# Performance work log

Hardware: AMD Instinct MI355X
Metric: run time of the kernel (lower is better)

The kernel has to match this reference:

```python
import jax, jax.numpy as jnp
import numpy as np

CHUNKS = 4
QMAX = 127.0

def fake_quant_int8(t):
    # per-tensor amax calibration -> symmetric int8 fake quant with STE
    amax = jnp.max(jnp.abs(t))
    scale = jnp.maximum(amax, 1e-12) / QMAX
    q = jnp.clip(jnp.round(t / scale), -128.0, 127.0) * scale
    return t + jax.lax.stop_gradient(q - t)

def conv2d(x, w):
    # NCHW x, OIHW w; stride 1, padding 1, dilation 1, groups 1
    return jax.lax.conv_general_dilated(
        x, w, window_strides=(1, 1), padding=((1, 1), (1, 1)),
        dimension_numbers=('NCHW', 'OIHW', 'NCHW'))

def setup_inputs() -> dict:
    key = jax.random.key(0)
    k1, k2, k3 = jax.random.split(key, 3)
    x = jax.random.normal(k1, (8, 256, 128, 128), dtype=jnp.float32)
    weight = jax.random.normal(k2, (512, 256, 3, 3), dtype=jnp.float32) * 0.05
    bias_data = jax.random.normal(k3, (512,), dtype=jnp.float32)
    return {'x': x, 'weight': weight, 'bias_data': bias_data}

def reference(x, weight, bias_data):
    # seg_mode='weight', opt_type='default': input quantized once,
    # weight chunked along out_channels, each chunk quantized separately.
    xq = fake_quant_int8(x)
    out_ch = weight.shape[0]
    csize = out_ch // CHUNKS
    outs = []
    for i in range(CHUNKS):
        w_chunk = weight[i * csize:(i + 1) * csize]
        wq = fake_quant_int8(w_chunk)
        outs.append(conv2d(xq, wq))
    res = jnp.concatenate(outs, axis=1)  # [B, out_ch, H, W]
    return res + bias_data[None, :, None, None]
```

## Files before the change

### kernel.cpp

```cpp
#include <hip/hip_runtime.h>
#include <hip/hip_bf16.h>


typedef int i32x4 __attribute__((ext_vector_type(4)));

__device__ __forceinline__ void llds16(const void* g, void* l) {
    __builtin_amdgcn_global_load_lds(
        (const __attribute__((address_space(1))) void*)g,
        (__attribute__((address_space(3))) void*)l,
        16, 0, 0);
}

__device__ __forceinline__ float f4max(float4 v) {
    return fmaxf(fmaxf(fabsf(v.x), fabsf(v.y)), fmaxf(fabsf(v.z), fabsf(v.w)));
}

__global__ __launch_bounds__(256) void k_amax(const float4* __restrict__ x,
                                              const float4* __restrict__ w4,
                                              float* __restrict__ part) {
    __shared__ float red[4];
    int t = threadIdx.x;
    float m = 0.f;
    if (blockIdx.x < 2048) {
        int tid = blockIdx.x * 256 + t;
        float4 v[16];
#pragma unroll
        for (int k = 0; k < 16; ++k)
            v[k] = x[(size_t)tid + (size_t)k * 524288];
#pragma unroll
        for (int k = 0; k < 16; ++k) m = fmaxf(m, f4max(v[k]));
    } else {
        int b = blockIdx.x - 2048;
        int chunk = b / 288;
        int tid = (b - chunk * 288) * 256 + t;
        m = f4max(w4[(size_t)chunk * 73728 + tid]);
    }
    for (int off = 32; off > 0; off >>= 1) m = fmaxf(m, __shfl_xor(m, off, 64));
    if ((t & 63) == 0) red[t >> 6] = m;
    __syncthreads();
    if (t == 0)
        part[blockIdx.x] = fmaxf(fmaxf(red[0], red[1]), fmaxf(red[2], red[3]));
}

__global__ __launch_bounds__(256) void k_amax2(const float* __restrict__ part,
                                               unsigned* __restrict__ amaxb) {
    __shared__ float red[4];
    int t = threadIdx.x;
    float m = 0.f;
#pragma unroll
    for (int k = 0; k < 8; ++k) m = fmaxf(m, part[t + k * 256]);
    for (int off = 32; off > 0; off >>= 1) m = fmaxf(m, __shfl_xor(m, off, 64));
    if ((t & 63) == 0) red[t >> 6] = m;
    __syncthreads();
    if (t == 0)
        amaxb[0] = __float_as_uint(fmaxf(fmaxf(red[0], red[1]), fmaxf(red[2], red[3])));
    int c = t >> 6, l = t & 63;
    float wm = 0.f;
#pragma unroll
    for (int k = 0; k < 5; ++k) {
        int i = l + k * 64;
        if (i < 288) wm = fmaxf(wm, part[2048 + c * 288 + i]);
    }
    for (int off = 32; off > 0; off >>= 1) wm = fmaxf(wm, __shfl_xor(wm, off, 64));
    if (l == 0) amaxb[1 + c] = __float_as_uint(wm);
}

__global__ __launch_bounds__(256) void k_quant_x(const float* __restrict__ x,
                                                 signed char* __restrict__ qx,
                                                 const unsigned* __restrict__ amaxb) {
    float inv = 127.0f / fmaxf(__uint_as_float(amaxb[0]), 1e-12f);
    int row = blockIdx.x;
    int n = row >> 7, h = row & 127;
    int t = threadIdx.x;
    int w4 = t & 31, cg = t >> 5;
    const float* base = x + (size_t)n * 256 * 16384 + (size_t)h * 128 + w4 * 4;
#pragma unroll
    for (int pp = 0; pp < 2; ++pp) {
        int c0 = pp * 128 + cg * 16;
        float4 v[16];
#pragma unroll
        for (int j = 0; j < 16; ++j)
            v[j] = *(const float4*)(base + (size_t)(c0 + j) * 16384);
#pragma unroll
        for (int i = 0; i < 4; ++i) {
            unsigned wds[4];
#pragma unroll
            for (int jg = 0; jg < 4; ++jg) {
                unsigned u = 0;
#pragma unroll
                for (int jj = 0; jj < 4; ++jj) {
                    float f = (&v[jg * 4 + jj].x)[i];
                    int q = (int)fminf(fmaxf(rintf(f * inv), -128.f), 127.f);
                    u |= ((unsigned)(q & 255)) << (8 * jj);
                }
                wds[jg] = u;
            }
            *(uint4*)&qx[(size_t)row * 32768 + (size_t)(w4 * 4 + i) * 256 + c0] =
                make_uint4(wds[0], wds[1], wds[2], wds[3]);
        }
    }
}

__global__ void k_quant_w(const float* __restrict__ wsrc, signed char* __restrict__ qw,
                          const unsigned* __restrict__ amaxb) {
    int idx = blockIdx.x * 256 + threadIdx.x;
    int oc = idx >> 8, c = idx & 255;
    float inv = 127.0f / fmaxf(__uint_as_float(amaxb[1 + (oc >> 7)]), 1e-12f);
    const float* src = wsrc + (size_t)idx * 9;
    float v[9];
#pragma unroll
    for (int rs = 0; rs < 9; ++rs) v[rs] = src[rs];
#pragma unroll
    for (int rs = 0; rs < 9; ++rs) {
        float qf = fminf(fmaxf(rintf(v[rs] * inv), -128.f), 127.f);
        qw[((size_t)(rs * 512 + oc)) * 256 + c] = (signed char)(int)qf;
    }
}

__global__ __launch_bounds__(256, 2) void k_conv(
    const signed char* __restrict__ qx, const signed char* __restrict__ qw,
    const signed char* __restrict__ zb, const unsigned* __restrict__ amaxb,
    const float* __restrict__ bias, float* __restrict__ out) {
    __shared__ __align__(16) signed char xs[4 * 8320];
    __shared__ __align__(16) signed char wt[3 * 128 * 64];
    int orig = blockIdx.x;
    int wgid = (orig & 7) * 256 + (orig >> 3);
    int rowpair = wgid >> 2, ocg = wgid & 3;
    int n = rowpair >> 6;
    int h0 = (rowpair & 63) * 2;
    int t = threadIdx.x, wid = t >> 6, lane = t & 63;
    int p = lane & 15, hi = lane >> 4;
    int rowsel = wid >> 1, whalf = wid & 1;

    i32x4 acc[8][4] = {};

    auto stageX = [&](int cb) {
#pragma unroll
        for (int i = 0; i < 9; ++i) {
            int idx = t + i * 256;
            if (idx < 2080) {
                int rowk = idx / 520;
                int j = idx - rowk * 520;
                int wr = j >> 2, q4 = j & 3;
                int wg = wr - 1;
                int hh = h0 - 1 + rowk;
                int q4s = q4 ^ ((wr >> 1) & 3);
                const signed char* src = (hh >= 0 && hh < 128 && wg >= 0 && wg < 128)
                    ? qx + (size_t)(n * 128 + hh) * 32768 + wg * 256 + cb * 64 + q4s * 16
                    : zb;
                llds16(src, xs + (size_t)(i * 256 + wid * 64) * 16);
            }
        }
    };
    auto stageW = [&](int cb, int r) {
#pragma unroll
        for (int i = 0; i < 6; ++i) {
            int idx = t + i * 256;
            int s = idx >> 9, rem = idx & 511;
            int oc = rem >> 2, q4 = rem & 3;
            int q4s = q4 ^ ((oc >> 1) & 3);
            const signed char* src = qw
                + (size_t)((r * 3 + s) * 512 + ocg * 128 + oc) * 256 + cb * 64 + q4s * 16;
            llds16(src, wt + (size_t)(i * 256 + wid * 64) * 16);
        }
    };

    for (int cb = 0; cb < 4; ++cb) {
#pragma unroll
        for (int r = 0; r < 3; ++r) {
            if (r == 0) stageX(cb);
            stageW(cb, r);
            __syncthreads();
            int rowk = r + rowsel;
#pragma unroll
            for (int s = 0; s < 3; ++s) {
                i32x4 a[8], b[4];
#pragma unroll
                for (int mf = 0; mf < 8; ++mf) {
                    int ocr = mf * 16 + p;
                    a[mf] = *(const i32x4*)&wt[s * 8192 + ocr * 64
                                               + ((hi ^ ((ocr >> 1) & 3)) << 4)];
                }
#pragma unroll
                for (int nf = 0; nf < 4; ++nf) {
                    int wrow = whalf * 64 + nf * 16 + p + s;
                    b[nf] = *(const i32x4*)&xs[rowk * 8320 + wrow * 64
                                               + ((hi ^ ((wrow >> 1) & 3)) << 4)];
                }
#pragma unroll
                for (int mf = 0; mf < 8; ++mf)
#pragma unroll
                    for (int nf = 0; nf < 4; ++nf)
                        acc[mf][nf] = __builtin_amdgcn_mfma_i32_16x16x64_i8(
                            a[mf], b[nf], acc[mf][nf], 0, 0, 0);
            }
            __syncthreads();
        }
    }

    float sx = fmaxf(__uint_as_float(amaxb[0]), 1e-12f) / 127.0f;
    float sw = fmaxf(__uint_as_float(amaxb[1 + ocg]), 1e-12f) / 127.0f;
    float sc = sx * sw;
    int h = h0 + rowsel;
#pragma unroll
    for (int mf = 0; mf < 8; ++mf)
#pragma unroll
        for (int nf = 0; nf < 4; ++nf)
#pragma unroll
            for (int j = 0; j < 4; ++j) {
                int oc = ocg * 128 + mf * 16 + hi * 4 + j;
                int px = whalf * 64 + nf * 16 + p;
                out[((size_t)(n * 512 + oc) * 128 + h) * 128 + px] =
                    (float)acc[mf][nf][j] * sc + bias[oc];
            }
}

extern "C" void kernel_launch(void* const* d_in, const int* in_sizes, int n_in,
                              void* d_out, int out_size, void* d_ws, size_t ws_size,
                              hipStream_t stream) {
    const float* x    = (const float*)d_in[0];
    const float* wgt  = (const float*)d_in[1];
    const float* bias = (const float*)d_in[2];
    float* out = (float*)d_out;

    unsigned* amaxb = (unsigned*)d_ws;
    float* part = (float*)((char*)d_ws + 256);
    signed char* qx = (signed char*)d_ws + 16384;
    signed char* qw = (signed char*)d_ws + 16384 + 33554432;
    const signed char* zb = (const signed char*)d_ws + 64;

    hipMemsetAsync(d_ws, 0, 256, stream);

    k_amax<<<3200, 256, 0, stream>>>((const float4*)x, (const float4*)wgt, part);
    k_amax2<<<1, 256, 0, stream>>>(part, amaxb);
    k_quant_x<<<1024, 256, 0, stream>>>(x, qx, amaxb);
    k_quant_w<<<512, 256, 0, stream>>>(wgt, qw, amaxb);
    k_conv<<<dim3(2048), 256, 0, stream>>>(qx, qw, zb, amaxb, bias, out);
}
```

Before: 224.2 us.

## Double-buffer conv LDS staging with 512-thread blocks over four output rows

The int8 conv kernel now runs 512-thread workgroups covering four output rows, so each block loads six input rows per channel block instead of four per two rows, which cuts halo re-reads. Input and weight tiles are double-buffered in LDS, with the next stage's global-to-LDS loads issued before computing the current one and gated by explicit vmcnt waits and raw s_barrier. Halo columns are zeroed once at the start, and MFMA sections are wrapped in s_setprio. LDS use roughly doubles, to about 148 KB per block, which may limit occupancy. The hand-tuned vmcnt counts are fragile and could race if they are off.

```diff
diff --git a/kernel.cpp b/kernel.cpp
--- a/kernel.cpp
+++ b/kernel.cpp
@@ -13,6 +13,12 @@
 
 __device__ __forceinline__ float f4max(float4 v) {
     return fmaxf(fmaxf(fabsf(v.x), fabsf(v.y)), fmaxf(fabsf(v.z), fabsf(v.w)));
+}
+
+__device__ __forceinline__ void barrier_f() {
+    asm volatile("" ::: "memory");
+    __builtin_amdgcn_s_barrier();
+    asm volatile("" ::: "memory");
 }
 
 __global__ __launch_bounds__(256) void k_amax(const float4* __restrict__ x,
@@ -117,85 +123,93 @@
     }
 }
 
-__global__ __launch_bounds__(256, 2) void k_conv(
+__global__ __launch_bounds__(512, 2) void k_conv(
     const signed char* __restrict__ qx, const signed char* __restrict__ qw,
     const signed char* __restrict__ zb, const unsigned* __restrict__ amaxb,
     const float* __restrict__ bias, float* __restrict__ out) {
-    __shared__ __align__(16) signed char xs[4 * 8320];
-    __shared__ __align__(16) signed char wt[3 * 128 * 64];
+    __shared__ __align__(16) signed char xs2[2 * 6 * 130 * 64];
+    __shared__ __align__(16) signed char wt2[2 * 3 * 128 * 64];
     int orig = blockIdx.x;
-    int wgid = (orig & 7) * 256 + (orig >> 3);
-    int rowpair = wgid >> 2, ocg = wgid & 3;
-    int n = rowpair >> 6;
-    int h0 = (rowpair & 63) * 2;
+    int wgid = (orig & 7) * 128 + (orig >> 3);
+    int n = wgid >> 7;
+    int rq = (wgid >> 2) & 31, ocg = wgid & 3;
+    int h0 = rq * 4;
     int t = threadIdx.x, wid = t >> 6, lane = t & 63;
-    int p = lane & 15, hi = lane >> 4;
+    int lp = lane & 15, hi = lane >> 4;
     int rowsel = wid >> 1, whalf = wid & 1;
 
     i32x4 acc[8][4] = {};
 
-    auto stageX = [&](int cb) {
-#pragma unroll
-        for (int i = 0; i < 9; ++i) {
-            int idx = t + i * 256;
-            if (idx < 2080) {
-                int rowk = idx / 520;
-                int j = idx - rowk * 520;
-                int wr = j >> 2, q4 = j & 3;
-                int wg = wr - 1;
-                int hh = h0 - 1 + rowk;
-                int q4s = q4 ^ ((wr >> 1) & 3);
-                const signed char* src = (hh >= 0 && hh < 128 && wg >= 0 && wg < 128)
-                    ? qx + (size_t)(n * 128 + hh) * 32768 + wg * 256 + cb * 64 + q4s * 16
-                    : zb;
-                llds16(src, xs + (size_t)(i * 256 + wid * 64) * 16);
-            }
+    auto stageX = [&](int cbx, int bufx) {
+#pragma unroll
+        for (int i = 0; i < 6; ++i) {
+            int hh = h0 - 1 + i;
+            int w = t >> 2, q4 = t & 3;
+            int q4s = q4 ^ (((w + 1) >> 1) & 3);
+            const signed char* src = (hh >= 0 && hh < 128)
+                ? qx + (size_t)(n * 128 + hh) * 32768 + w * 256 + cbx * 64 + q4s * 16
+                : zb;
+            llds16(src, xs2 + (size_t)bufx * 49920 + i * 8320 + 64 + t * 16);
         }
     };
-    auto stageW = [&](int cb, int r) {
-#pragma unroll
-        for (int i = 0; i < 6; ++i) {
-            int idx = t + i * 256;
-            int s = idx >> 9, rem = idx & 511;
-            int oc = rem >> 2, q4 = rem & 3;
+    auto stageW = [&](int cbw, int rw, int bufw) {
+#pragma unroll
+        for (int i = 0; i < 3; ++i) {
+            int oc = t >> 2, q4 = t & 3;
             int q4s = q4 ^ ((oc >> 1) & 3);
             const signed char* src = qw
-                + (size_t)((r * 3 + s) * 512 + ocg * 128 + oc) * 256 + cb * 64 + q4s * 16;
-            llds16(src, wt + (size_t)(i * 256 + wid * 64) * 16);
+                + (size_t)((rw * 3 + i) * 512 + ocg * 128 + oc) * 256 + cbw * 64 + q4s * 16;
+            llds16(src, wt2 + (size_t)bufw * 24576 + i * 8192 + t * 16);
         }
     };
 
-    for (int cb = 0; cb < 4; ++cb) {
-#pragma unroll
-        for (int r = 0; r < 3; ++r) {
-            if (r == 0) stageX(cb);
-            stageW(cb, r);
-            __syncthreads();
-            int rowk = r + rowsel;
-#pragma unroll
-            for (int s = 0; s < 3; ++s) {
-                i32x4 a[8], b[4];
-#pragma unroll
-                for (int mf = 0; mf < 8; ++mf) {
-                    int ocr = mf * 16 + p;
-                    a[mf] = *(const i32x4*)&wt[s * 8192 + ocr * 64
-                                               + ((hi ^ ((ocr >> 1) & 3)) << 4)];
-                }
-#pragma unroll
-                for (int nf = 0; nf < 4; ++nf) {
-                    int wrow = whalf * 64 + nf * 16 + p + s;
-                    b[nf] = *(const i32x4*)&xs[rowk * 8320 + wrow * 64
-                                               + ((hi ^ ((wrow >> 1) & 3)) << 4)];
-                }
-#pragma unroll
-                for (int mf = 0; mf < 8; ++mf)
-#pragma unroll
-                    for (int nf = 0; nf < 4; ++nf)
-                        acc[mf][nf] = __builtin_amdgcn_mfma_i32_16x16x64_i8(
-                            a[mf], b[nf], acc[mf][nf], 0, 0, 0);
-            }
-            __syncthreads();
-        }
+    if (t < 96) {
+        int unit = t >> 2, q = t & 3;
+        int buf = unit / 12, rem = unit % 12;
+        int rowk = rem >> 1, side = rem & 1;
+        *(i32x4*)&xs2[(size_t)buf * 49920 + rowk * 8320 + (side ? 129 : 0) * 64 + q * 16] =
+            i32x4{0, 0, 0, 0};
+    }
+    stageX(0, 0);
+    stageW(0, 0, 0);
+    asm volatile("s_waitcnt lgkmcnt(0)" ::: "memory");
+    barrier_f();
+
+#pragma unroll
+    for (int p = 0; p < 12; ++p) {
+        const int r = p % 3, cb = p / 3;
+        if (p < 11) stageW((p + 1) / 3, (p + 1) % 3, (p + 1) & 1);
+        if (r == 1 && cb < 3) stageX(cb + 1, (cb + 1) & 1);
+        if (p == 11)      asm volatile("s_waitcnt vmcnt(0)" ::: "memory");
+        else if (r == 0 || p == 10) asm volatile("s_waitcnt vmcnt(3)" ::: "memory");
+        else              asm volatile("s_waitcnt vmcnt(9)" ::: "memory");
+        barrier_f();
+        const int wb = p & 1, xb = cb & 1, rowk = r + rowsel;
+#pragma unroll
+        for (int s = 0; s < 3; ++s) {
+            i32x4 a[8], b[4];
+#pragma unroll
+            for (int mf = 0; mf < 8; ++mf) {
+                int ocr = mf * 16 + lp;
+                a[mf] = *(const i32x4*)&wt2[(size_t)wb * 24576 + s * 8192 + ocr * 64
+                                            + ((hi ^ ((ocr >> 1) & 3)) << 4)];
+            }
+#pragma unroll
+            for (int nf = 0; nf < 4; ++nf) {
+                int slot = whalf * 64 + nf * 16 + lp + s;
+                b[nf] = *(const i32x4*)&xs2[(size_t)xb * 49920 + rowk * 8320 + slot * 64
+                                            + ((hi ^ ((slot >> 1) & 3)) << 4)];
+            }
+            __builtin_amdgcn_s_setprio(1);
+#pragma unroll
+            for (int mf = 0; mf < 8; ++mf)
+#pragma unroll
+                for (int nf = 0; nf < 4; ++nf)
+                    acc[mf][nf] = __builtin_amdgcn_mfma_i32_16x16x64_i8(
+                        a[mf], b[nf], acc[mf][nf], 0, 0, 0);
+            __builtin_amdgcn_s_setprio(0);
+        }
+        barrier_f();
     }
 
     float sx = fmaxf(__uint_as_float(amaxb[0]), 1e-12f) / 127.0f;
@@ -209,7 +223,7 @@
 #pragma unroll
             for (int j = 0; j < 4; ++j) {
                 int oc = ocg * 128 + mf * 16 + hi * 4 + j;
-                int px = whalf * 64 + nf * 16 + p;
+                int px = whalf * 64 + nf * 16 + lp;
                 out[((size_t)(n * 512 + oc) * 128 + h) * 128 + px] =
                     (float)acc[mf][nf][j] * sc + bias[oc];
             }
@@ -235,5 +249,5 @@
     k_amax2<<<1, 256, 0, stream>>>(part, amaxb);
     k_quant_x<<<1024, 256, 0, stream>>>(x, qx, amaxb);
     k_quant_w<<<512, 256, 0, stream>>>(wgt, qw, amaxb);
-    k_conv<<<dim3(2048), 256, 0, stream>>>(qx, qw, zb, amaxb, bias, out);
-}
+    k_conv<<<dim3(1024), 512, 0, stream>>>(qx, qw, zb, amaxb, bias, out);
+}
```

Result: slower. 242.0 us (+7.9%).

## Double-buffer per-tap weight tiles and raise occupancy in int8 conv

Applied to the files above, without the earlier changes.

Replaces the three-tap weight staging per kernel row with a two-slot double buffer holding one 3x3 tap at a time. The next tap's weights are prefetched into LDS while the current tap's MFMAs run, and launch bounds rise from 2 to 3 blocks per CU because LDS use drops. The input tile is still loaded synchronously at each channel-block boundary. The cost is more barriers, one per tap instead of one per row, and the higher occupancy target may squeeze the 128 accumulator registers per thread and cause spills.

```diff
diff --git a/kernel.cpp b/kernel.cpp
--- a/kernel.cpp
+++ b/kernel.cpp
@@ -117,19 +117,19 @@
     }
 }
 
-__global__ __launch_bounds__(256, 2) void k_conv(
+__global__ __launch_bounds__(256, 3) void k_conv(
     const signed char* __restrict__ qx, const signed char* __restrict__ qw,
     const signed char* __restrict__ zb, const unsigned* __restrict__ amaxb,
     const float* __restrict__ bias, float* __restrict__ out) {
     __shared__ __align__(16) signed char xs[4 * 8320];
-    __shared__ __align__(16) signed char wt[3 * 128 * 64];
+    __shared__ __align__(16) signed char wt[2][128 * 64];
     int orig = blockIdx.x;
     int wgid = (orig & 7) * 256 + (orig >> 3);
     int rowpair = wgid >> 2, ocg = wgid & 3;
     int n = rowpair >> 6;
     int h0 = (rowpair & 63) * 2;
     int t = threadIdx.x, wid = t >> 6, lane = t & 63;
-    int p = lane & 15, hi = lane >> 4;
+    int lp = lane & 15, hi = lane >> 4;
     int rowsel = wid >> 1, whalf = wid & 1;
 
     i32x4 acc[8][4] = {};
@@ -152,49 +152,54 @@
             }
         }
     };
-    auto stageW = [&](int cb, int r) {
-#pragma unroll
-        for (int i = 0; i < 6; ++i) {
+    auto stageW1 = [&](int P, int buf) {
+        int cb = P / 9, rs = P % 9;
+#pragma unroll
+        for (int i = 0; i < 2; ++i) {
             int idx = t + i * 256;
-            int s = idx >> 9, rem = idx & 511;
-            int oc = rem >> 2, q4 = rem & 3;
+            int oc = idx >> 2, q4 = idx & 3;
             int q4s = q4 ^ ((oc >> 1) & 3);
             const signed char* src = qw
-                + (size_t)((r * 3 + s) * 512 + ocg * 128 + oc) * 256 + cb * 64 + q4s * 16;
-            llds16(src, wt + (size_t)(i * 256 + wid * 64) * 16);
+                + (size_t)(rs * 512 + ocg * 128 + oc) * 256 + cb * 64 + q4s * 16;
+            llds16(src, &wt[buf][0] + (size_t)idx * 16);
         }
     };
 
+    stageX(0);
+    stageW1(0, 0);
+    __syncthreads();
+
     for (int cb = 0; cb < 4; ++cb) {
 #pragma unroll
-        for (int r = 0; r < 3; ++r) {
-            if (r == 0) stageX(cb);
-            stageW(cb, r);
+        for (int rs = 0; rs < 9; ++rs) {
+            int P = cb * 9 + rs;
+            if (P < 35) stageW1(P + 1, (P + 1) & 1);
+            int r = rs / 3, s = rs - r * 3;
+            int rowk = r + rowsel;
+            i32x4 a[8], b[4];
+#pragma unroll
+            for (int mf = 0; mf < 8; ++mf) {
+                int ocr = mf * 16 + lp;
+                a[mf] = *(const i32x4*)&wt[P & 1][ocr * 64
+                                                  + ((hi ^ ((ocr >> 1) & 3)) << 4)];
+            }
+#pragma unroll
+            for (int nf = 0; nf < 4; ++nf) {
+                int slot = whalf * 64 + nf * 16 + lp + s;
+                b[nf] = *(const i32x4*)&xs[rowk * 8320 + slot * 64
+                                           + ((hi ^ ((slot >> 1) & 3)) << 4)];
+            }
+#pragma unroll
+            for (int mf = 0; mf < 8; ++mf)
+#pragma unroll
+                for (int nf = 0; nf < 4; ++nf)
+                    acc[mf][nf] = __builtin_amdgcn_mfma_i32_16x16x64_i8(
+                        a[mf], b[nf], acc[mf][nf], 0, 0, 0);
             __syncthreads();
-            int rowk = r + rowsel;
-#pragma unroll
-            for (int s = 0; s < 3; ++s) {
-                i32x4 a[8], b[4];
-#pragma unroll
-                for (int mf = 0; mf < 8; ++mf) {
-                    int ocr = mf * 16 + p;
-                    a[mf] = *(const i32x4*)&wt[s * 8192 + ocr * 64
-                                               + ((hi ^ ((ocr >> 1) & 3)) << 4)];
-                }
-#pragma unroll
-                for (int nf = 0; nf < 4; ++nf) {
-                    int wrow = whalf * 64 + nf * 16 + p + s;
-                    b[nf] = *(const i32x4*)&xs[rowk * 8320 + wrow * 64
-                                               + ((hi ^ ((wrow >> 1) & 3)) << 4)];
-                }
-#pragma unroll
-                for (int mf = 0; mf < 8; ++mf)
-#pragma unroll
-                    for (int nf = 0; nf < 4; ++nf)
-                        acc[mf][nf] = __builtin_amdgcn_mfma_i32_16x16x64_i8(
-                            a[mf], b[nf], acc[mf][nf], 0, 0, 0);
-            }
-            __syncthreads();
+            if (rs == 8 && cb < 3) {
+                stageX(cb + 1);
+                __syncthreads();
+            }
         }
     }
 
@@ -209,7 +214,7 @@
 #pragma unroll
             for (int j = 0; j < 4; ++j) {
                 int oc = ocg * 128 + mf * 16 + hi * 4 + j;
-                int px = whalf * 64 + nf * 16 + p;
+                int px = whalf * 64 + nf * 16 + lp;
                 out[((size_t)(n * 512 + oc) * 128 + h) * 128 + px] =
                     (float)acc[mf][nf][j] * sc + bias[oc];
             }
```

Result: slower. 433.9 us (+93.5%).

## Switch conv MFMA to 32x32x32 int8 tiles with double-buffered LDS fragment reads

Applied to the files above, without the earlier changes.

Replaces the 16x16x64 int8 MFMA tiling, an 8x4 grid of fragments per wave, with 32x32x32 int8 MFMA on a 4x2 grid. This cuts the number of LDS fragment reads per unit of math and the number of MFMA issues. The K loop over the 3 kernel columns is split into six half-K steps, and A/B fragments are loaded ahead into two register sets so LDS reads overlap with MFMA execution. The epilogue index mapping is updated for the 32x32 accumulator layout. Accumulator register count stays the same, but the extra prefetch buffers may raise register pressure under the 2-waves-per-SIMD launch bound.

```diff
diff --git a/kernel.cpp b/kernel.cpp
--- a/kernel.cpp
+++ b/kernel.cpp
@@ -3,6 +3,7 @@
 
 
 typedef int i32x4 __attribute__((ext_vector_type(4)));
+typedef int i32x16 __attribute__((ext_vector_type(16)));
 
 __device__ __forceinline__ void llds16(const void* g, void* l) {
     __builtin_amdgcn_global_load_lds(
@@ -129,10 +130,10 @@
     int n = rowpair >> 6;
     int h0 = (rowpair & 63) * 2;
     int t = threadIdx.x, wid = t >> 6, lane = t & 63;
-    int p = lane & 15, hi = lane >> 4;
+    int l31 = lane & 31, hi2 = lane >> 5;
     int rowsel = wid >> 1, whalf = wid & 1;
 
-    i32x4 acc[8][4] = {};
+    i32x16 acc[4][2] = {};
 
     auto stageX = [&](int cb) {
 #pragma unroll
@@ -164,6 +165,34 @@
             llds16(src, wt + (size_t)(i * 256 + wid * 64) * 16);
         }
     };
+    auto rdA = [&](int u, i32x4* a) {
+        int s = u >> 1, ks = u & 1;
+        int q = ks * 2 + hi2;
+#pragma unroll
+        for (int mf = 0; mf < 4; ++mf) {
+            int ocr = mf * 32 + l31;
+            a[mf] = *(const i32x4*)&wt[s * 8192 + ocr * 64
+                                       + ((q ^ ((ocr >> 1) & 3)) << 4)];
+        }
+    };
+    auto rdB = [&](int u, int rowk, i32x4* b) {
+        int s = u >> 1, ks = u & 1;
+        int q = ks * 2 + hi2;
+#pragma unroll
+        for (int nf = 0; nf < 2; ++nf) {
+            int slot = whalf * 64 + nf * 32 + l31 + s;
+            b[nf] = *(const i32x4*)&xs[rowk * 8320 + slot * 64
+                                       + ((q ^ ((slot >> 1) & 3)) << 4)];
+        }
+    };
+    auto domm = [&](i32x4* a, i32x4* b) {
+#pragma unroll
+        for (int mf = 0; mf < 4; ++mf)
+#pragma unroll
+            for (int nf = 0; nf < 2; ++nf)
+                acc[mf][nf] = __builtin_amdgcn_mfma_i32_32x32x32_i8(
+                    a[mf], b[nf], acc[mf][nf], 0, 0, 0);
+    };
 
     for (int cb = 0; cb < 4; ++cb) {
 #pragma unroll
@@ -172,28 +201,19 @@
             stageW(cb, r);
             __syncthreads();
             int rowk = r + rowsel;
-#pragma unroll
-            for (int s = 0; s < 3; ++s) {
-                i32x4 a[8], b[4];
-#pragma unroll
-                for (int mf = 0; mf < 8; ++mf) {
-                    int ocr = mf * 16 + p;
-                    a[mf] = *(const i32x4*)&wt[s * 8192 + ocr * 64
-                                               + ((hi ^ ((ocr >> 1) & 3)) << 4)];
-                }
-#pragma unroll
-                for (int nf = 0; nf < 4; ++nf) {
-                    int wrow = whalf * 64 + nf * 16 + p + s;
-                    b[nf] = *(const i32x4*)&xs[rowk * 8320 + wrow * 64
-                                               + ((hi ^ ((wrow >> 1) & 3)) << 4)];
-                }
-#pragma unroll
-                for (int mf = 0; mf < 8; ++mf)
-#pragma unroll
-                    for (int nf = 0; nf < 4; ++nf)
-                        acc[mf][nf] = __builtin_amdgcn_mfma_i32_16x16x64_i8(
-                            a[mf], b[nf], acc[mf][nf], 0, 0, 0);
-            }
+            i32x4 aP[4], bP[2], aQ[4], bQ[2];
+            rdA(0, aP); rdB(0, rowk, bP);
+            rdA(1, aQ); rdB(1, rowk, bQ);
+            domm(aP, bP);
+            rdA(2, aP); rdB(2, rowk, bP);
+            domm(aQ, bQ);
+            rdA(3, aQ); rdB(3, rowk, bQ);
+            domm(aP, bP);
+            rdA(4, aP); rdB(4, rowk, bP);
+            domm(aQ, bQ);
+            rdA(5, aQ); rdB(5, rowk, bQ);
+            domm(aP, bP);
+            domm(aQ, bQ);
             __syncthreads();
         }
     }
@@ -203,13 +223,13 @@
     float sc = sx * sw;
     int h = h0 + rowsel;
 #pragma unroll
-    for (int mf = 0; mf < 8; ++mf)
-#pragma unroll
-        for (int nf = 0; nf < 4; ++nf)
-#pragma unroll
-            for (int j = 0; j < 4; ++j) {
-                int oc = ocg * 128 + mf * 16 + hi * 4 + j;
-                int px = whalf * 64 + nf * 16 + p;
+    for (int mf = 0; mf < 4; ++mf)
+#pragma unroll
+        for (int nf = 0; nf < 2; ++nf)
+#pragma unroll
+            for (int j = 0; j < 16; ++j) {
+                int oc = ocg * 128 + mf * 32 + (j & 3) + 8 * (j >> 2) + 4 * hi2;
+                int px = whalf * 64 + nf * 32 + l31;
                 out[((size_t)(n * 512 + oc) * 128 + h) * 128 + px] =
                     (float)acc[mf][nf][j] * sc + bias[oc];
             }
```

Measured after the change: 246.6 us. +10.0%, slower.
